# Performance work log

Measured on AMD Instinct MI355X. Metric: run time of the kernel, lower is better.

## Reference

```python
import jax, jax.numpy as jnp
import numpy as np

BS, N, D, B, D_PM = 8, 4096, 1024, 8, 64
BUDGET = 16.0


def setup_inputs() -> dict:
    key = jax.random.key(0)
    ks = jax.random.split(key, 6)
    H = jax.random.normal(ks[0], (BS, N, D), jnp.float32)
    surprise = jax.random.normal(ks[1], (BS, N, D), jnp.float32)
    # W_pm initialized as (1/B)*I + small noise, as in initialize()
    eye = jnp.eye(D_PM, dtype=jnp.float32)
    W_pm = eye / B + 0.01 * jax.random.normal(ks[2], (BS, B, D_PM, D_PM), jnp.float32)
    proj_in_w = jax.random.normal(ks[3], (D_PM, D), jnp.float32) / np.float32(np.sqrt(D))
    proj_in_b = jnp.zeros((D_PM,), jnp.float32)
    # original zero-inits proj_out; use small values so output is non-trivial
    proj_out_w = 0.02 * jax.random.normal(ks[4], (D, D_PM), jnp.float32)
    proj_out_b = jnp.zeros((D,), jnp.float32)
    raw_beta = jnp.full((B,), -3.0, jnp.float32)
    raw_decay = jnp.full((B,), np.float32(np.log(0.999 / 0.001)), jnp.float32)  # logit(0.999)
    surp_scale = jnp.ones((1,), jnp.float32)
    surp_bias = jnp.zeros((1,), jnp.float32)
    return dict(H=H, surprise=surprise, W_pm=W_pm,
                proj_in_w=proj_in_w, proj_in_b=proj_in_b,
                proj_out_w=proj_out_w, proj_out_b=proj_out_b,
                raw_beta=raw_beta, raw_decay=raw_decay,
                surp_scale=surp_scale, surp_bias=surp_bias)


def reference(H, surprise, W_pm, proj_in_w, proj_in_b, proj_out_w, proj_out_b,
              raw_beta, raw_decay, surp_scale, surp_bias):
    # ---- read ----
    pre = jnp.einsum('bnd,pd->bnp', H, proj_in_w) + proj_in_b          # [BS,N,D_pm]
    W_sum = jnp.sum(W_pm, axis=1)                                      # [BS,D_pm,D_pm]
    post = jnp.einsum('bnp,bqp->bnq', pre, W_sum)                      # pre @ W_sum^T
    pm_read = jnp.einsum('bnq,dq->bnd', post, proj_out_w) + proj_out_b # [BS,N,D]
    # ---- commit (Hebbian, surprise-gated) ----
    surp_mag = jnp.linalg.norm(surprise, axis=-1)                      # [BS,N]
    s = jax.nn.sigmoid(surp_scale * surp_mag + surp_bias)              # [BS,N]
    weighted = jnp.sqrt(s)[..., None] * pre                            # [BS,N,D_pm]
    G = jnp.einsum('bnp,bnq->bpq', weighted, weighted) / N             # [BS,D_pm,D_pm]
    beta = jax.nn.softplus(raw_beta)                                   # [B]
    decay = jax.nn.sigmoid(raw_decay)                                  # [B]
    eye = jnp.eye(D_PM, dtype=pre.dtype)
    T = decay[None, :, None, None] * eye + beta[None, :, None, None] * G[:, None]  # [BS,B,D_pm,D_pm]
    W_new = jnp.einsum('bkij,bkjq->bkiq', W_pm, T)                     # [BS,B,D_pm,D_pm]
    frob = jnp.sqrt(jnp.sum(W_new * W_new, axis=(-2, -1), keepdims=True))
    scale = jnp.minimum(BUDGET / jnp.maximum(frob, 1e-8), 1.0)
    W_new = W_new * scale
    return pm_read, W_new
```

## Files before the change

kernel.cpp:

```cpp
#include <hip/hip_runtime.h>

typedef unsigned short u16;
typedef __attribute__((ext_vector_type(4))) float f32x4;
typedef __attribute__((ext_vector_type(8))) short s16x8;

static constexpr int N_ = 4096;
static constexpr int D_ = 1024;

__device__ __forceinline__ u16 f2bf(float f) {
  unsigned u = __float_as_uint(f);
  u += 0x7FFFu + ((u >> 16) & 1u);
  return (u16)(u >> 16);
}

__device__ __forceinline__ f32x4 zero4() {
  f32x4 z; z[0] = 0.f; z[1] = 0.f; z[2] = 0.f; z[3] = 0.f; return z;
}

__global__ __launch_bounds__(256) void k_prep(
    const float* __restrict__ Wpm, const float* __restrict__ piw,
    const float* __restrict__ pw, u16* __restrict__ WpB,
    u16* __restrict__ PowB, u16* __restrict__ WsumB) {
  int bid = blockIdx.x, tid = threadIdx.x;
  if (bid < 8) {
    for (int idx = tid; idx < 4096; idx += 256) {
      float s = 0.f;
#pragma unroll
      for (int k = 0; k < 8; ++k)
        s += Wpm[((size_t)(bid * 8 + k)) * 4096 + idx];
      WsumB[bid * 4096 + idx] = f2bf(s);
    }
  } else if (bid < 24) {
    size_t i0 = (size_t)(bid - 8) * 4096;
    for (int idx = tid; idx < 4096; idx += 256)
      WpB[i0 + idx] = f2bf(piw[i0 + idx]);
  } else {
    size_t i0 = (size_t)(bid - 24) * 4096;
    for (int idx = tid; idx < 4096; idx += 256)
      PowB[i0 + idx] = f2bf(pw[i0 + idx]);
  }
}

__global__ __launch_bounds__(256) void k_main(
    const float* __restrict__ H, const float* __restrict__ Sur,
    const float* __restrict__ pib, const float* __restrict__ pob,
    const float* __restrict__ sscale_p, const float* __restrict__ sbias_p,
    const u16* __restrict__ WpB, const u16* __restrict__ PowB,
    const u16* __restrict__ WsumB, float* __restrict__ Gacc,
    float* __restrict__ out) {
  __shared__ u16 preRP[64][72];
  __shared__ u16 wRP[64][72];
  __shared__ u16 postRP[64][72];
  __shared__ float sqs[64];

  const int tid = threadIdx.x;
  const int lane = tid & 63;
  const int w = tid >> 6;
  const int llo = lane & 15;
  const int lhi = lane >> 4;
  const int b = blockIdx.x >> 6;
  const int row0 = (blockIdx.x & 63) * 64;

  const float sscale = sscale_p[0];
  const float sbias = sbias_p[0];

  {
    const float* sbase = Sur + ((size_t)b * N_ + row0) * D_;
    for (int i = 0; i < 16; ++i) {
      int r = w * 16 + i;
      const float* p = sbase + (size_t)r * D_ + lane * 4;
      float a = 0.f;
#pragma unroll
      for (int j = 0; j < 4; ++j) {
        float4 v = *(const float4*)(p + j * 256);
        a += v.x * v.x + v.y * v.y + v.z * v.z + v.w * v.w;
      }
#pragma unroll
      for (int m = 1; m < 64; m <<= 1) a += __shfl_xor(a, m, 64);
      if (lane == 0) {
        float mag = sqrtf(a);
        float s = 1.f / (1.f + __expf(-(sscale * mag + sbias)));
        sqs[r] = sqrtf(s);
      }
    }
  }
  __syncthreads();

  f32x4 accA[4];
#pragma unroll
  for (int t = 0; t < 4; ++t) accA[t] = zero4();
  {
    const float* hrow =
        H + ((size_t)b * N_ + row0 + w * 16 + llo) * D_ + lhi * 8;
    const u16* wp0 = WpB + (size_t)llo * 1024 + lhi * 8;
#pragma unroll 2
    for (int k0 = 0; k0 < 1024; k0 += 32) {
      float4 a0 = *(const float4*)(hrow + k0);
      float4 a1 = *(const float4*)(hrow + k0 + 4);
      s16x8 af;
      af[0] = (short)f2bf(a0.x); af[1] = (short)f2bf(a0.y);
      af[2] = (short)f2bf(a0.z); af[3] = (short)f2bf(a0.w);
      af[4] = (short)f2bf(a1.x); af[5] = (short)f2bf(a1.y);
      af[6] = (short)f2bf(a1.z); af[7] = (short)f2bf(a1.w);
#pragma unroll
      for (int t = 0; t < 4; ++t) {
        s16x8 bf = *(const s16x8*)(wp0 + (size_t)t * 16 * 1024 + k0);
        accA[t] = __builtin_amdgcn_mfma_f32_16x16x32_bf16(af, bf, accA[t], 0, 0, 0);
      }
    }
  }
#pragma unroll
  for (int t = 0; t < 4; ++t) {
    float bias = pib[t * 16 + llo];
#pragma unroll
    for (int r = 0; r < 4; ++r) {
      int rr = w * 16 + lhi * 4 + r;
      float v = accA[t][r] + bias;
      preRP[rr][t * 16 + llo] = f2bf(v);
      wRP[rr][t * 16 + llo] = f2bf(v * sqs[rr]);
    }
  }
  __syncthreads();

  {
    f32x4 accG[4];
#pragma unroll
    for (int t = 0; t < 4; ++t) accG[t] = zero4();
#pragma unroll
    for (int k0 = 0; k0 < 64; k0 += 32) {
      s16x8 ag;
#pragma unroll
      for (int j = 0; j < 8; ++j)
        ag[j] = (short)wRP[k0 + lhi * 8 + j][w * 16 + llo];
#pragma unroll
      for (int t = 0; t < 4; ++t) {
        s16x8 bg;
#pragma unroll
        for (int j = 0; j < 8; ++j)
          bg[j] = (short)wRP[k0 + lhi * 8 + j][t * 16 + llo];
        accG[t] = __builtin_amdgcn_mfma_f32_16x16x32_bf16(ag, bg, accG[t], 0, 0, 0);
      }
    }
    float* gb = Gacc + (size_t)b * 4096;
#pragma unroll
    for (int t = 0; t < 4; ++t)
#pragma unroll
      for (int r = 0; r < 4; ++r)
        atomicAdd(gb + (w * 16 + lhi * 4 + r) * 64 + t * 16 + llo, accG[t][r]);
  }

  {
    f32x4 accC[4];
#pragma unroll
    for (int t = 0; t < 4; ++t) accC[t] = zero4();
    const u16* wsb = WsumB + (size_t)b * 4096;
#pragma unroll
    for (int k0 = 0; k0 < 64; k0 += 32) {
      s16x8 ac = *(const s16x8*)&preRP[w * 16 + llo][k0 + lhi * 8];
#pragma unroll
      for (int t = 0; t < 4; ++t) {
        s16x8 bc = *(const s16x8*)(wsb + (size_t)(t * 16 + llo) * 64 + k0 + lhi * 8);
        accC[t] = __builtin_amdgcn_mfma_f32_16x16x32_bf16(ac, bc, accC[t], 0, 0, 0);
      }
    }
#pragma unroll
    for (int t = 0; t < 4; ++t)
#pragma unroll
      for (int r = 0; r < 4; ++r)
        postRP[w * 16 + lhi * 4 + r][t * 16 + llo] = f2bf(accC[t][r]);
  }
  __syncthreads();

  {
    s16x8 ad0 = *(const s16x8*)&postRP[w * 16 + llo][lhi * 8];
    s16x8 ad1 = *(const s16x8*)&postRP[w * 16 + llo][32 + lhi * 8];
    float* orow = out + ((size_t)b * N_ + row0 + w * 16) * D_;
    for (int n0 = 0; n0 < 1024; n0 += 16) {
      s16x8 b0 = *(const s16x8*)(PowB + (size_t)(n0 + llo) * 64 + lhi * 8);
      s16x8 b1 = *(const s16x8*)(PowB + (size_t)(n0 + llo) * 64 + 32 + lhi * 8);
      f32x4 acc = zero4();
      acc = __builtin_amdgcn_mfma_f32_16x16x32_bf16(ad0, b0, acc, 0, 0, 0);
      acc = __builtin_amdgcn_mfma_f32_16x16x32_bf16(ad1, b1, acc, 0, 0, 0);
      float bias = pob[n0 + llo];
#pragma unroll
      for (int r = 0; r < 4; ++r)
        orow[(size_t)(lhi * 4 + r) * D_ + n0 + llo] = acc[r] + bias;
    }
  }
}

__global__ __launch_bounds__(256) void k_wnew(
    const float* __restrict__ Wpm, const float* __restrict__ Gacc,
    const float* __restrict__ rbeta, const float* __restrict__ rdecay,
    float* __restrict__ outW) {
  __shared__ float Wk[64][66];
  __shared__ float Gl[64][66];
  __shared__ float red[4];
  int bk = blockIdx.x;
  int b = bk >> 3, k = bk & 7;
  int tid = threadIdx.x;
  const float* wsrc = Wpm + (size_t)bk * 4096;
  const float* gsrc = Gacc + (size_t)b * 4096;
  for (int idx = tid; idx < 4096; idx += 256) {
    Wk[idx >> 6][idx & 63] = wsrc[idx];
    Gl[idx >> 6][idx & 63] = gsrc[idx];
  }
  __syncthreads();
  float beta = log1pf(__expf(rbeta[k]));
  float decay = 1.f / (1.f + __expf(-rdecay[k]));
  float bn = beta * (1.f / 4096.f);
  int q = tid & 63;
  int rbase = tid >> 6;
  float vals[16];
  float ss = 0.f;
#pragma unroll
  for (int i = 0; i < 16; ++i) {
    int row = i * 4 + rbase;
    float acc = 0.f;
#pragma unroll 8
    for (int j = 0; j < 64; ++j) acc += Wk[row][j] * Gl[j][q];
    float v = decay * Wk[row][q] + bn * acc;
    vals[i] = v;
    ss += v * v;
  }
#pragma unroll
  for (int m = 1; m < 64; m <<= 1) ss += __shfl_xor(ss, m, 64);
  if ((tid & 63) == 0) red[tid >> 6] = ss;
  __syncthreads();
  float frob = sqrtf(red[0] + red[1] + red[2] + red[3]);
  float scale = fminf(16.f / fmaxf(frob, 1e-8f), 1.f);
  float* dst = outW + (size_t)bk * 4096;
#pragma unroll
  for (int i = 0; i < 16; ++i) dst[i * 256 + tid] = vals[i] * scale;
}

extern "C" void kernel_launch(void* const* d_in, const int* in_sizes, int n_in,
                              void* d_out, int out_size, void* d_ws, size_t ws_size,
                              hipStream_t stream) {
  const float* H      = (const float*)d_in[0];
  const float* Sur    = (const float*)d_in[1];
  const float* Wpm    = (const float*)d_in[2];
  const float* piw    = (const float*)d_in[3];
  const float* pib    = (const float*)d_in[4];
  const float* pw     = (const float*)d_in[5];
  const float* pob    = (const float*)d_in[6];
  const float* rbeta  = (const float*)d_in[7];
  const float* rdecay = (const float*)d_in[8];
  const float* sscale = (const float*)d_in[9];
  const float* sbias  = (const float*)d_in[10];
  float* out = (float*)d_out;

  char* ws = (char*)d_ws;
  float* Gacc = (float*)(ws);
  u16* WsumB  = (u16*)(ws + 131072);
  u16* WpB    = (u16*)(ws + 196608);
  u16* PowB   = (u16*)(ws + 327680);

  hipMemsetAsync(Gacc, 0, 131072, stream);
  k_prep<<<40, 256, 0, stream>>>(Wpm, piw, pw, WpB, PowB, WsumB);
  k_main<<<512, 256, 0, stream>>>(H, Sur, pib, pob, sscale, sbias,
                                  WpB, PowB, WsumB, Gacc, out);
  k_wnew<<<64, 256, 0, stream>>>(Wpm, Gacc, rbeta, rdecay,
                                 out + (size_t)8 * 4096 * 1024);
}
```

Before: 146.5 us.

## Fold W_sum into output projection and split K across eight waves

```diff
diff --git a/kernel.cpp b/kernel.cpp
--- a/kernel.cpp
+++ b/kernel.cpp
@@ -20,81 +20,89 @@
 __global__ __launch_bounds__(256) void k_prep(
     const float* __restrict__ Wpm, const float* __restrict__ piw,
     const float* __restrict__ pw, u16* __restrict__ WpB,
-    u16* __restrict__ PowB, u16* __restrict__ WsumB) {
+    u16* __restrict__ MB) {
   int bid = blockIdx.x, tid = threadIdx.x;
-  if (bid < 8) {
-    for (int idx = tid; idx < 4096; idx += 256) {
-      float s = 0.f;
-#pragma unroll
-      for (int k = 0; k < 8; ++k)
-        s += Wpm[((size_t)(bid * 8 + k)) * 4096 + idx];
-      WsumB[bid * 4096 + idx] = f2bf(s);
-    }
-  } else if (bid < 24) {
-    size_t i0 = (size_t)(bid - 8) * 4096;
+  if (bid < 16) {
+    size_t i0 = (size_t)bid * 4096;
     for (int idx = tid; idx < 4096; idx += 256)
       WpB[i0 + idx] = f2bf(piw[i0 + idx]);
-  } else {
-    size_t i0 = (size_t)(bid - 24) * 4096;
-    for (int idx = tid; idx < 4096; idx += 256)
-      PowB[i0 + idx] = f2bf(pw[i0 + idx]);
-  }
-}
-
-__global__ __launch_bounds__(256) void k_main(
+    return;
+  }
+  __shared__ float Ws[64][65];
+  int idx2 = bid - 16;
+  int b = idx2 >> 4, t = idx2 & 15;
+  for (int idx = tid; idx < 4096; idx += 256) {
+    float s = 0.f;
+#pragma unroll
+    for (int k = 0; k < 8; ++k)
+      s += Wpm[((size_t)(b * 8 + k)) * 4096 + idx];
+    Ws[idx >> 6][idx & 63] = s;
+  }
+  __syncthreads();
+  u16* mb = MB + ((size_t)b << 16);
+  for (int oidx = tid; oidx < 4096; oidx += 256) {
+    int r = oidx >> 6, c = oidx & 63;
+    int drow = t * 64 + r;
+    const float* prow = pw + (size_t)drow * 64;
+    float acc = 0.f;
+#pragma unroll 8
+    for (int q = 0; q < 64; ++q) acc += prow[q] * Ws[q][c];
+    mb[(size_t)drow * 64 + c] = f2bf(acc);
+  }
+}
+
+__global__ __launch_bounds__(512, 4) void k_main(
     const float* __restrict__ H, const float* __restrict__ Sur,
     const float* __restrict__ pib, const float* __restrict__ pob,
     const float* __restrict__ sscale_p, const float* __restrict__ sbias_p,
-    const u16* __restrict__ WpB, const u16* __restrict__ PowB,
-    const u16* __restrict__ WsumB, float* __restrict__ Gacc,
-    float* __restrict__ out) {
+    const u16* __restrict__ WpB, const u16* __restrict__ MB,
+    float* __restrict__ Gacc, float* __restrict__ out) {
+  __shared__ float preF[64][68];
   __shared__ u16 preRP[64][72];
   __shared__ u16 wRP[64][72];
-  __shared__ u16 postRP[64][72];
   __shared__ float sqs[64];
 
   const int tid = threadIdx.x;
   const int lane = tid & 63;
   const int w = tid >> 6;
+  const int wm = w & 3;
+  const int wk = w >> 2;
   const int llo = lane & 15;
   const int lhi = lane >> 4;
   const int b = blockIdx.x >> 6;
   const int row0 = (blockIdx.x & 63) * 64;
 
-  const float sscale = sscale_p[0];
-  const float sbias = sbias_p[0];
-
-  {
-    const float* sbase = Sur + ((size_t)b * N_ + row0) * D_;
-    for (int i = 0; i < 16; ++i) {
-      int r = w * 16 + i;
-      const float* p = sbase + (size_t)r * D_ + lane * 4;
-      float a = 0.f;
-#pragma unroll
-      for (int j = 0; j < 4; ++j) {
-        float4 v = *(const float4*)(p + j * 256);
-        a += v.x * v.x + v.y * v.y + v.z * v.z + v.w * v.w;
-      }
-#pragma unroll
-      for (int m = 1; m < 64; m <<= 1) a += __shfl_xor(a, m, 64);
-      if (lane == 0) {
-        float mag = sqrtf(a);
-        float s = 1.f / (1.f + __expf(-(sscale * mag + sbias)));
-        sqs[r] = sqrtf(s);
-      }
-    }
-  }
-  __syncthreads();
+  {
+    int r = w * 8 + (lane >> 3);
+    const float* p = Sur + ((size_t)b * N_ + row0 + r) * D_ + (lane & 7) * 4;
+    float a0 = 0.f, a1 = 0.f;
+#pragma unroll 8
+    for (int j = 0; j < 32; j += 2) {
+      float4 v = *(const float4*)(p + j * 32);
+      float4 v2 = *(const float4*)(p + j * 32 + 32);
+      a0 += v.x * v.x + v.y * v.y + v.z * v.z + v.w * v.w;
+      a1 += v2.x * v2.x + v2.y * v2.y + v2.z * v2.z + v2.w * v2.w;
+    }
+    float a = a0 + a1;
+    a += __shfl_xor(a, 1, 64);
+    a += __shfl_xor(a, 2, 64);
+    a += __shfl_xor(a, 4, 64);
+    if ((lane & 7) == 0) {
+      float mag = sqrtf(a);
+      float s = 1.f / (1.f + __expf(-(sscale_p[0] * mag + sbias_p[0])));
+      sqs[r] = sqrtf(s);
+    }
+  }
 
   f32x4 accA[4];
 #pragma unroll
   for (int t = 0; t < 4; ++t) accA[t] = zero4();
   {
     const float* hrow =
-        H + ((size_t)b * N_ + row0 + w * 16 + llo) * D_ + lhi * 8;
-    const u16* wp0 = WpB + (size_t)llo * 1024 + lhi * 8;
+        H + ((size_t)b * N_ + row0 + wm * 16 + llo) * D_ + wk * 512 + lhi * 8;
+    const u16* wp0 = WpB + (size_t)llo * 1024 + wk * 512 + lhi * 8;
 #pragma unroll 2
-    for (int k0 = 0; k0 < 1024; k0 += 32) {
+    for (int k0 = 0; k0 < 512; k0 += 32) {
       float4 a0 = *(const float4*)(hrow + k0);
       float4 a1 = *(const float4*)(hrow + k0 + 4);
       s16x8 af;
@@ -109,15 +117,25 @@
       }
     }
   }
-#pragma unroll
-  for (int t = 0; t < 4; ++t) {
-    float bias = pib[t * 16 + llo];
-#pragma unroll
-    for (int r = 0; r < 4; ++r) {
-      int rr = w * 16 + lhi * 4 + r;
-      float v = accA[t][r] + bias;
-      preRP[rr][t * 16 + llo] = f2bf(v);
-      wRP[rr][t * 16 + llo] = f2bf(v * sqs[rr]);
+  if (wk == 1) {
+#pragma unroll
+    for (int t = 0; t < 4; ++t)
+#pragma unroll
+      for (int r = 0; r < 4; ++r)
+        preF[wm * 16 + lhi * 4 + r][t * 16 + llo] = accA[t][r];
+  }
+  __syncthreads();
+  if (wk == 0) {
+#pragma unroll
+    for (int t = 0; t < 4; ++t) {
+      float bias = pib[t * 16 + llo];
+#pragma unroll
+      for (int r = 0; r < 4; ++r) {
+        int row = wm * 16 + lhi * 4 + r;
+        float v = accA[t][r] + preF[row][t * 16 + llo] + bias;
+        preRP[row][t * 16 + llo] = f2bf(v);
+        wRP[row][t * 16 + llo] = f2bf(v * sqs[row]);
+      }
     }
   }
   __syncthreads();
@@ -126,58 +144,36 @@
     f32x4 accG[4];
 #pragma unroll
     for (int t = 0; t < 4; ++t) accG[t] = zero4();
-#pragma unroll
-    for (int k0 = 0; k0 < 64; k0 += 32) {
-      s16x8 ag;
+    int kbase = wk * 32;
+    s16x8 ag;
+#pragma unroll
+    for (int j = 0; j < 8; ++j)
+      ag[j] = (short)wRP[kbase + lhi * 8 + j][wm * 16 + llo];
+#pragma unroll
+    for (int t = 0; t < 4; ++t) {
+      s16x8 bg;
 #pragma unroll
       for (int j = 0; j < 8; ++j)
-        ag[j] = (short)wRP[k0 + lhi * 8 + j][w * 16 + llo];
-#pragma unroll
-      for (int t = 0; t < 4; ++t) {
-        s16x8 bg;
-#pragma unroll
-        for (int j = 0; j < 8; ++j)
-          bg[j] = (short)wRP[k0 + lhi * 8 + j][t * 16 + llo];
-        accG[t] = __builtin_amdgcn_mfma_f32_16x16x32_bf16(ag, bg, accG[t], 0, 0, 0);
-      }
+        bg[j] = (short)wRP[kbase + lhi * 8 + j][t * 16 + llo];
+      accG[t] = __builtin_amdgcn_mfma_f32_16x16x32_bf16(ag, bg, accG[t], 0, 0, 0);
     }
     float* gb = Gacc + (size_t)b * 4096;
 #pragma unroll
     for (int t = 0; t < 4; ++t)
 #pragma unroll
       for (int r = 0; r < 4; ++r)
-        atomicAdd(gb + (w * 16 + lhi * 4 + r) * 64 + t * 16 + llo, accG[t][r]);
-  }
-
-  {
-    f32x4 accC[4];
-#pragma unroll
-    for (int t = 0; t < 4; ++t) accC[t] = zero4();
-    const u16* wsb = WsumB + (size_t)b * 4096;
-#pragma unroll
-    for (int k0 = 0; k0 < 64; k0 += 32) {
-      s16x8 ac = *(const s16x8*)&preRP[w * 16 + llo][k0 + lhi * 8];
-#pragma unroll
-      for (int t = 0; t < 4; ++t) {
-        s16x8 bc = *(const s16x8*)(wsb + (size_t)(t * 16 + llo) * 64 + k0 + lhi * 8);
-        accC[t] = __builtin_amdgcn_mfma_f32_16x16x32_bf16(ac, bc, accC[t], 0, 0, 0);
-      }
-    }
-#pragma unroll
-    for (int t = 0; t < 4; ++t)
-#pragma unroll
-      for (int r = 0; r < 4; ++r)
-        postRP[w * 16 + lhi * 4 + r][t * 16 + llo] = f2bf(accC[t][r]);
-  }
-  __syncthreads();
-
-  {
-    s16x8 ad0 = *(const s16x8*)&postRP[w * 16 + llo][lhi * 8];
-    s16x8 ad1 = *(const s16x8*)&postRP[w * 16 + llo][32 + lhi * 8];
-    float* orow = out + ((size_t)b * N_ + row0 + w * 16) * D_;
-    for (int n0 = 0; n0 < 1024; n0 += 16) {
-      s16x8 b0 = *(const s16x8*)(PowB + (size_t)(n0 + llo) * 64 + lhi * 8);
-      s16x8 b1 = *(const s16x8*)(PowB + (size_t)(n0 + llo) * 64 + 32 + lhi * 8);
+        atomicAdd(gb + (wm * 16 + lhi * 4 + r) * 64 + t * 16 + llo, accG[t][r]);
+  }
+
+  {
+    s16x8 ad0 = *(const s16x8*)&preRP[wm * 16 + llo][lhi * 8];
+    s16x8 ad1 = *(const s16x8*)&preRP[wm * 16 + llo][32 + lhi * 8];
+    const u16* mb = MB + ((size_t)b << 16);
+    float* orow = out + ((size_t)b * N_ + row0 + wm * 16) * D_;
+    int nend = wk * 512 + 512;
+    for (int n0 = wk * 512; n0 < nend; n0 += 16) {
+      s16x8 b0 = *(const s16x8*)(mb + (size_t)(n0 + llo) * 64 + lhi * 8);
+      s16x8 b1 = *(const s16x8*)(mb + (size_t)(n0 + llo) * 64 + 32 + lhi * 8);
       f32x4 acc = zero4();
       acc = __builtin_amdgcn_mfma_f32_16x16x32_bf16(ad0, b0, acc, 0, 0, 0);
       acc = __builtin_amdgcn_mfma_f32_16x16x32_bf16(ad1, b1, acc, 0, 0, 0);
@@ -252,14 +248,13 @@
 
   char* ws = (char*)d_ws;
   float* Gacc = (float*)(ws);
-  u16* WsumB  = (u16*)(ws + 131072);
-  u16* WpB    = (u16*)(ws + 196608);
-  u16* PowB   = (u16*)(ws + 327680);
+  u16* WpB    = (u16*)(ws + 131072);
+  u16* MB     = (u16*)(ws + 262144);
 
   hipMemsetAsync(Gacc, 0, 131072, stream);
-  k_prep<<<40, 256, 0, stream>>>(Wpm, piw, pw, WpB, PowB, WsumB);
-  k_main<<<512, 256, 0, stream>>>(H, Sur, pib, pob, sscale, sbias,
-                                  WpB, PowB, WsumB, Gacc, out);
+  k_prep<<<144, 256, 0, stream>>>(Wpm, piw, pw, WpB, MB);
+  k_main<<<512, 512, 0, stream>>>(H, Sur, pib, pob, sscale, sbias,
+                                  WpB, MB, Gacc, out);
   k_wnew<<<64, 256, 0, stream>>>(Wpm, Gacc, rbeta, rdecay,
                                  out + (size_t)8 * 4096 * 1024);
 }
```

Result: slower. 165.6 us (+13.1%).
